# Performance work log

Measured on AMD Instinct MI355X. Metric: run time of the kernel, lower is better.

## Reference

```python
import jax, jax.numpy as jnp
import numpy as np

B, K, D = 16384, 512, 64

def _lin(k, fan_in, shape):
    return jax.random.normal(k, shape, jnp.float32) * (1.0 / np.sqrt(fan_in))

def setup_inputs() -> dict:
    key = jax.random.key(0)
    ks = jax.random.split(key, 12)
    return {
        'X':  jax.random.normal(ks[0], (B, 1, 28, 28), jnp.float32),
        'W1': _lin(ks[1], 784, (784, 1000)),  'b1': jnp.zeros((1000,), jnp.float32),
        'W2': _lin(ks[2], 1000, (1000, 500)), 'b2': jnp.zeros((500,), jnp.float32),
        'W3': _lin(ks[3], 500, (500, 300)),   'b3': jnp.zeros((300,), jnp.float32),
        'W4': _lin(ks[4], 300, (300, D)),     'b4': jnp.zeros((D,), jnp.float32),
        'E':  jax.random.normal(ks[5], (K, D), jnp.float32),
        'V1': _lin(ks[6], D, (D, 300)),       'c1': jnp.zeros((300,), jnp.float32),
        'V2': _lin(ks[7], 300, (300, 500)),   'c2': jnp.zeros((500,), jnp.float32),
        'V3': _lin(ks[8], 500, (500, 1000)),  'c3': jnp.zeros((1000,), jnp.float32),
        'V4': _lin(ks[9], 1000, (1000, 784)), 'c4': jnp.zeros((784,), jnp.float32),
    }

def find_nearest(query, target):
    # Euclidean nearest row of `target` for each row of `query`.
    # Expanded form ||q||^2 + ||t||^2 - 2 q.t ; argmin of d2 == argmin of sqrt(d2).
    d2 = (jnp.sum(query * query, axis=1, keepdims=True)
          + jnp.sum(target * target, axis=1)[None, :]
          - 2.0 * query @ target.T)                      # [Nq, Nt]
    idx = jnp.argmin(d2, axis=1)
    return target[idx]

def reference(X, W1, b1, W2, b2, W3, b3, W4, b4, E,
              V1, c1, V2, c2, V3, c3, V4, c4):
    x = X.reshape(-1, 784)
    h = jax.nn.relu(x @ W1 + b1)
    h = jax.nn.relu(h @ W2 + b2)
    h = jax.nn.relu(h @ W3 + b3)
    Z_enc = h @ W4 + b4                                   # [B, D]
    Z_dec = find_nearest(Z_enc, E)                        # [B, D] gathered codebook rows
    g = jax.nn.leaky_relu(Z_dec @ V1 + c1, 0.1)
    g = jax.nn.leaky_relu(g @ V2 + c2, 0.1)
    g = jax.nn.leaky_relu(g @ V3 + c3, 0.1)
    X_recon = jnp.tanh(g @ V4 + c4).reshape(-1, 1, 28, 28)
    Z_enc_for_embd = find_nearest(E, Z_enc)               # [K, D] gathered encoder rows
    return (X_recon, Z_enc, Z_dec, Z_enc_for_embd)
```

## Files before the change

kernel.cpp:

```cpp
#include <hip/hip_runtime.h>
#include <hip/hip_bf16.h>


typedef __attribute__((ext_vector_type(8))) short short8v;
typedef __attribute__((ext_vector_type(4))) float f32x4;

__device__ inline ushort f2bf(float v) {
    __hip_bfloat16 h = __float2bfloat16(v);
    return *reinterpret_cast<ushort*>(&h);
}
__device__ inline float bf2f(ushort s) {
    __hip_bfloat16 h;
    *reinterpret_cast<ushort*>(&h) = s;
    return __bfloat162float(h);
}

__device__ __forceinline__ void stage_tile(const ushort* __restrict__ src,
                                           ushort* dst, int wid, int lane)
{
#pragma unroll
    for (int j = 0; j < 2; ++j) {
        const int ci = (j << 2) + wid;
        __builtin_amdgcn_global_load_lds(
            (const __attribute__((address_space(1))) unsigned int*)(src + ci * 512 + lane * 8),
            (__attribute__((address_space(3))) unsigned int*)(dst + ci * 512),
            16, 0, 0);
    }
}

template<int ACT, bool SPLIT, int OMODE>
__global__ __launch_bounds__(256)
void gemm_mfma(const ushort* __restrict__ At, const ushort* __restrict__ Alt,
               const ushort* __restrict__ Bt, const ushort* __restrict__ Blt,
               const float* __restrict__ bias,
               float* __restrict__ Cf, ushort* __restrict__ Chi, ushort* __restrict__ Clo,
               int kbgA, int nsteps, int N)
{
    __shared__ short8v AhV[512];
    __shared__ short8v BhV[512];
    __shared__ short8v AlV[SPLIT ? 512 : 1];
    __shared__ short8v BlV[SPLIT ? 512 : 1];
    ushort* Ah = (ushort*)AhV;
    ushort* Bh = (ushort*)BhV;
    ushort* Al = (ushort*)AlV;
    ushort* Bl = (ushort*)BlV;

    const int tid  = threadIdx.x;
    const int lane = tid & 63;
    const int wid  = tid >> 6;
    const int wr   = (wid >> 1) * 64;
    const int wc   = (wid & 1) * 64;

    const int flat = blockIdx.y * gridDim.x + blockIdx.x;
    const int cpx  = (gridDim.x * gridDim.y) >> 3;
    const int swz  = (flat & 7) * cpx + (flat >> 3);
    const int cb   = swz % gridDim.x;
    const int rb   = swz / gridDim.x;
    const int row0 = rb * 128;
    const int col0 = cb * 128;

    f32x4 acc[4][4];
#pragma unroll
    for (int m = 0; m < 4; ++m)
#pragma unroll
        for (int n = 0; n < 4; ++n) acc[m][n] = (f32x4){0.f, 0.f, 0.f, 0.f};

    const int fr = lane & 15;
    const int kq = lane >> 4;

    const size_t abase = (size_t)rb * kbgA * 1024;
    const size_t bbase = (size_t)cb * kbgA * 1024;

    for (int s = 0; s < nsteps; ++s) {
        const size_t off = (size_t)s * 4096;
        stage_tile(At + abase + off, Ah, wid, lane);
        stage_tile(Bt + bbase + off, Bh, wid, lane);
        if (SPLIT) {
            stage_tile(Alt + abase + off, Al, wid, lane);
            stage_tile(Blt + bbase + off, Bl, wid, lane);
        }
        __syncthreads();

        short8v a_h[4], b_h[4], a_l[4], b_l[4];
#pragma unroll
        for (int m = 0; m < 4; ++m) {
            a_h[m] = *(const short8v*)&Ah[kq * 1024 + (wr + m * 16 + fr) * 8];
            if (SPLIT) a_l[m] = *(const short8v*)&Al[kq * 1024 + (wr + m * 16 + fr) * 8];
        }
#pragma unroll
        for (int n = 0; n < 4; ++n) {
            b_h[n] = *(const short8v*)&Bh[kq * 1024 + (wc + n * 16 + fr) * 8];
            if (SPLIT) b_l[n] = *(const short8v*)&Bl[kq * 1024 + (wc + n * 16 + fr) * 8];
        }
#pragma unroll
        for (int m = 0; m < 4; ++m)
#pragma unroll
            for (int n = 0; n < 4; ++n) {
                acc[m][n] = __builtin_amdgcn_mfma_f32_16x16x32_bf16(a_h[m], b_h[n], acc[m][n], 0, 0, 0);
                if (SPLIT) {
                    acc[m][n] = __builtin_amdgcn_mfma_f32_16x16x32_bf16(a_h[m], b_l[n], acc[m][n], 0, 0, 0);
                    acc[m][n] = __builtin_amdgcn_mfma_f32_16x16x32_bf16(a_l[m], b_h[n], acc[m][n], 0, 0, 0);
                }
            }
        __syncthreads();
    }

    const int kbgN = gridDim.x << 4;
#pragma unroll
    for (int n = 0; n < 4; ++n) {
        const int c = col0 + wc + n * 16 + fr;
        const float bv = (bias && c < N) ? bias[c] : 0.f;
#pragma unroll
        for (int m = 0; m < 4; ++m) {
#pragma unroll
            for (int i = 0; i < 4; ++i) {
                const int r = row0 + wr + m * 16 + kq * 4 + i;
                float v = acc[m][n][i] + bv;
                if (ACT == 1) v = fmaxf(v, 0.f);
                else if (ACT == 2) v = (v > 0.f) ? v : 0.1f * v;
                else if (ACT == 3) v = tanhf(v);
                if (OMODE == 0) {
                    if (c < N) Cf[(size_t)r * N + c] = v;
                } else {
                    if (c >= N) v = 0.f;
                    const size_t oi = (((size_t)(r >> 7) * kbgN + (c >> 3)) * 128 + (r & 127)) * 8 + (c & 7);
                    const ushort h = f2bf(v);
                    Chi[oi] = h;
                    if (OMODE == 2) Clo[oi] = f2bf(v - bf2f(h));
                }
            }
        }
    }
}

__global__ __launch_bounds__(256)
void gemm_f32_bt(const float* __restrict__ A, const float* __restrict__ W,
                 float* __restrict__ C, int M, int K, int N)
{
    __shared__ float As[16][68];
    __shared__ float Ws[16][68];

    const int tid = threadIdx.x;
    const int tx = tid & 15, ty = tid >> 4;
    const int row0 = blockIdx.y * 64, col0 = blockIdx.x * 64;

    float acc[4][4];
#pragma unroll
    for (int i = 0; i < 4; ++i)
#pragma unroll
        for (int j = 0; j < 4; ++j) acc[i][j] = 0.f;

    const int a_row = tid >> 2, a_k4 = (tid & 3) << 2;
    const int t_col = tid >> 2, t_k4 = (tid & 3) << 2;

    for (int k0 = 0; k0 < K; k0 += 16) {
        {
            const int gr = row0 + a_row, gk = k0 + a_k4;
            float4 av = *reinterpret_cast<const float4*>(A + (size_t)gr * K + gk);
            As[a_k4 + 0][a_row] = av.x; As[a_k4 + 1][a_row] = av.y;
            As[a_k4 + 2][a_row] = av.z; As[a_k4 + 3][a_row] = av.w;
        }
        {
            const int gc = col0 + t_col, gk = k0 + t_k4;
            float4 wv = *reinterpret_cast<const float4*>(W + (size_t)gc * K + gk);
            Ws[t_k4 + 0][t_col] = wv.x; Ws[t_k4 + 1][t_col] = wv.y;
            Ws[t_k4 + 2][t_col] = wv.z; Ws[t_k4 + 3][t_col] = wv.w;
        }
        __syncthreads();
#pragma unroll
        for (int kk = 0; kk < 16; ++kk) {
            float4 a = *reinterpret_cast<const float4*>(&As[kk][ty << 2]);
            float4 w = *reinterpret_cast<const float4*>(&Ws[kk][tx << 2]);
            acc[0][0] += a.x * w.x; acc[0][1] += a.x * w.y; acc[0][2] += a.x * w.z; acc[0][3] += a.x * w.w;
            acc[1][0] += a.y * w.x; acc[1][1] += a.y * w.y; acc[1][2] += a.y * w.z; acc[1][3] += a.y * w.w;
            acc[2][0] += a.z * w.x; acc[2][1] += a.z * w.y; acc[2][2] += a.z * w.z; acc[2][3] += a.z * w.w;
            acc[3][0] += a.w * w.x; acc[3][1] += a.w * w.y; acc[3][2] += a.w * w.z; acc[3][3] += a.w * w.w;
        }
        __syncthreads();
    }
#pragma unroll
    for (int i = 0; i < 4; ++i) {
        const int r = row0 + (ty << 2) + i;
#pragma unroll
        for (int j = 0; j < 4; ++j) {
            const int c = col0 + (tx << 2) + j;
            C[(size_t)r * N + c] = acc[i][j];
        }
    }
}

__global__ void row_norms64(const float* __restrict__ X, float* __restrict__ out, int rows)
{
    int r = blockIdx.x * blockDim.x + threadIdx.x;
    if (r >= rows) return;
    const float* p = X + (size_t)r * 64;
    float s = 0.f;
#pragma unroll
    for (int i = 0; i < 16; ++i) {
        float4 v = *reinterpret_cast<const float4*>(p + i * 4);
        s += v.x * v.x + v.y * v.y + v.z * v.z + v.w * v.w;
    }
    out[r] = s;
}

__global__ __launch_bounds__(256)
void argmin_rows(const float* __restrict__ S, const float* __restrict__ En2,
                 const float* __restrict__ E, float* __restrict__ Zdec,
                 ushort* __restrict__ Zdcb)
{
    const int wave = (blockIdx.x * blockDim.x + threadIdx.x) >> 6;
    const int lane = threadIdx.x & 63;
    if (wave >= 16384) return;
    const float* Srow = S + (size_t)wave * 512;
    float best = INFINITY;
    int bidx = 0x7fffffff;
    for (int k = lane; k < 512; k += 64) {
        float v = En2[k] - 2.0f * Srow[k];
        if (v < best) { best = v; bidx = k; }
    }
#pragma unroll
    for (int off = 32; off > 0; off >>= 1) {
        float ov = __shfl_down(best, off);
        int   oi = __shfl_down(bidx, off);
        if (ov < best || (ov == best && oi < bidx)) { best = ov; bidx = oi; }
    }
    bidx = __shfl(bidx, 0);
    const float val = E[(size_t)bidx * 64 + lane];
    Zdec[(size_t)wave * 64 + lane] = val;
    const size_t oi = (((size_t)(wave >> 7) * 8 + (lane >> 3)) * 128 + (wave & 127)) * 8 + (lane & 7);
    Zdcb[oi] = f2bf(val);
}

__global__ __launch_bounds__(256)
void argmin_cols_p1(const float* __restrict__ S, const float* __restrict__ Zn2,
                    float* __restrict__ pval, int* __restrict__ pidx)
{
    const int g   = blockIdx.x;
    const int tid = threadIdx.x;
    const int r0  = g << 6;
    float b0 = INFINITY, b1 = INFINITY;
    int   i0 = 0, i1 = 0;
    for (int r = 0; r < 64; ++r) {
        const float zn = Zn2[r0 + r];
        const float* row = S + (size_t)(r0 + r) * 512;
        const float v0 = zn - 2.0f * row[tid];
        const float v1 = zn - 2.0f * row[tid + 256];
        if (v0 < b0) { b0 = v0; i0 = r0 + r; }
        if (v1 < b1) { b1 = v1; i1 = r0 + r; }
    }
    pval[(size_t)tid * 256 + g]         = b0;
    pidx[(size_t)tid * 256 + g]         = i0;
    pval[(size_t)(tid + 256) * 256 + g] = b1;
    pidx[(size_t)(tid + 256) * 256 + g] = i1;
}

__global__ __launch_bounds__(256)
void argmin_cols_p2(const float* __restrict__ pval, const int* __restrict__ pidx,
                    const float* __restrict__ Zenc, float* __restrict__ Zemb)
{
    const int k   = blockIdx.x;
    const int tid = threadIdx.x;
    float v = pval[(size_t)k * 256 + tid];
    int   i = pidx[(size_t)k * 256 + tid];
    __shared__ float vs[256];
    __shared__ int   is_[256];
    vs[tid] = v; is_[tid] = i;
    __syncthreads();
    for (int s = 128; s > 0; s >>= 1) {
        if (tid < s) {
            if (vs[tid + s] < vs[tid] ||
                (vs[tid + s] == vs[tid] && is_[tid + s] < is_[tid])) {
                vs[tid] = vs[tid + s]; is_[tid] = is_[tid + s];
            }
        }
        __syncthreads();
    }
    const int idx = is_[0];
    if (tid < 64) Zemb[(size_t)k * 64 + tid] = Zenc[(size_t)idx * 64 + tid];
}

__global__ void conv_x(const float* __restrict__ X, ushort* __restrict__ hi,
                       ushort* __restrict__ lo)
{
    const long total = 128L * 100 * 1024;
    for (long idx = blockIdx.x * 256L + threadIdx.x; idx < total; idx += (long)gridDim.x * 256L) {
        const int j  = (int)(idx & 7);
        const long t = idx >> 3;
        const int rn = (int)(t & 127);
        const long u = t >> 7;
        const int kb = (int)(u % 100);
        const int rb = (int)(u / 100);
        const int r = rb * 128 + rn;
        const int k = kb * 8 + j;
        const float v = (k < 784) ? X[(size_t)r * 784 + k] : 0.f;
        const ushort h = f2bf(v);
        hi[idx] = h;
        lo[idx] = f2bf(v - bf2f(h));
    }
}

template<bool SPLIT>
__global__ void prep_w(const float* __restrict__ W, ushort* __restrict__ hi,
                       ushort* __restrict__ lo, int K, int N, int kbgTot, int npanels)
{
    const long total = (long)npanels * kbgTot * 1024;
    for (long idx = blockIdx.x * 256L + threadIdx.x; idx < total; idx += (long)gridDim.x * 256L) {
        const int j  = (int)(idx & 7);
        const long t = idx >> 3;
        const int cn = (int)(t & 127);
        const long u = t >> 7;
        const int kb = (int)(u % kbgTot);
        const int p  = (int)(u / kbgTot);
        const int k = kb * 8 + j;
        const int n = p * 128 + cn;
        const float v = (k < K && n < N) ? W[(size_t)k * N + n] : 0.f;
        const ushort h = f2bf(v);
        hi[idx] = h;
        if (SPLIT) lo[idx] = f2bf(v - bf2f(h));
    }
}

extern "C" void kernel_launch(void* const* d_in, const int* in_sizes, int n_in,
                              void* d_out, int out_size, void* d_ws, size_t ws_size,
                              hipStream_t stream)
{
    const float* X  = (const float*)d_in[0];
    const float* W1 = (const float*)d_in[1];
    const float* b1 = (const float*)d_in[2];
    const float* W2 = (const float*)d_in[3];
    const float* b2 = (const float*)d_in[4];
    const float* W3 = (const float*)d_in[5];
    const float* b3 = (const float*)d_in[6];
    const float* W4 = (const float*)d_in[7];
    const float* b4 = (const float*)d_in[8];
    const float* E  = (const float*)d_in[9];
    const float* V1 = (const float*)d_in[10];
    const float* c1 = (const float*)d_in[11];
    const float* V2 = (const float*)d_in[12];
    const float* c2 = (const float*)d_in[13];
    const float* V3 = (const float*)d_in[14];
    const float* c3 = (const float*)d_in[15];
    const float* V4 = (const float*)d_in[16];
    const float* c4 = (const float*)d_in[17];

    float* out  = (float*)d_out;
    float* Xrec = out;
    float* Zenc = out + 12845056;
    float* Zdec = out + 13893632;
    float* Zemb = out + 14942208;

    char* ws = (char*)d_ws;
    ushort* Xhi = (ushort*)(ws + 0);
    ushort* Xlo = (ushort*)(ws + 26214400);
    ushort* h2h = (ushort*)(ws + 0);
    ushort* h2l = (ushort*)(ws + 16777216);
    float*  S   = (float*)(ws + 0);
    ushort* g3  = (ushort*)(ws + 0);
    ushort* h1l = (ushort*)(ws + 52428800);
    ushort* h3h = (ushort*)(ws + 52428800);
    ushort* h3l = (ushort*)(ws + 65011712);
    ushort* g1  = (ushort*)(ws + 52428800);
    ushort* g2  = (ushort*)(ws + 65011712);
    ushort* h1h = (ushort*)d_out;
    float*  Zn2  = (float*)(ws + 85983232);
    float*  En2  = (float*)(ws + 86048768);
    ushort* Zdcb = (ushort*)(ws + 86050816);
    ushort* Wt1h = (ushort*)(ws + 88147968);
    ushort* Wt1l = (ushort*)(ws + 89786368);
    ushort* Wt2h = (ushort*)(ws + 91424768);
    ushort* Wt2l = (ushort*)(ws + 92473344);
    ushort* Wt3h = (ushort*)(ws + 93521920);
    ushort* Wt3l = (ushort*)(ws + 93915136);
    ushort* Wt4h = (ushort*)(ws + 94308352);
    ushort* Wt4l = (ushort*)(ws + 94406656);
    ushort* Vt1  = (ushort*)(ws + 94504960);
    ushort* Vt2  = (ushort*)(ws + 94554112);
    ushort* Vt3  = (ushort*)(ws + 94947328);
    ushort* Vt4  = (ushort*)(ws + 95995904);
    float*  Pv   = (float*)(ws + 97830912);
    int*    Pi   = (int*)  (ws + 98355200);

    const dim3 blk(256);

    conv_x<<<dim3(2048), blk, 0, stream>>>(X, Xhi, Xlo);
    prep_w<true ><<<dim3(256), blk, 0, stream>>>(W1, Wt1h, Wt1l, 784, 1000, 100, 8);
    prep_w<true ><<<dim3(256), blk, 0, stream>>>(W2, Wt2h, Wt2l, 1000, 500, 128, 4);
    prep_w<true ><<<dim3(128), blk, 0, stream>>>(W3, Wt3h, Wt3l, 500, 300, 64, 3);
    prep_w<true ><<<dim3(64),  blk, 0, stream>>>(W4, Wt4h, Wt4l, 300, 64, 48, 1);
    prep_w<false><<<dim3(64),  blk, 0, stream>>>(V1, Vt1, nullptr, 64, 300, 8, 3);
    prep_w<false><<<dim3(128), blk, 0, stream>>>(V2, Vt2, nullptr, 300, 500, 48, 4);
    prep_w<false><<<dim3(256), blk, 0, stream>>>(V3, Vt3, nullptr, 500, 1000, 64, 8);
    prep_w<false><<<dim3(256), blk, 0, stream>>>(V4, Vt4, nullptr, 1000, 784, 128, 7);

    gemm_mfma<1, true, 2><<<dim3(8, 128), blk, 0, stream>>>(Xhi, Xlo, Wt1h, Wt1l, b1, nullptr, h1h, h1l, 100, 25, 1000);
    gemm_mfma<1, true, 2><<<dim3(4, 128), blk, 0, stream>>>(h1h, h1l, Wt2h, Wt2l, b2, nullptr, h2h, h2l, 128, 32, 500);
    gemm_mfma<1, true, 2><<<dim3(3, 128), blk, 0, stream>>>(h2h, h2l, Wt3h, Wt3l, b3, nullptr, h3h, h3l, 64, 16, 300);
    gemm_mfma<0, true, 0><<<dim3(1, 128), blk, 0, stream>>>(h3h, h3l, Wt4h, Wt4l, b4, Zenc, nullptr, nullptr, 48, 12, 64);

    row_norms64<<<dim3(8),  dim3(64), 0, stream>>>(E,    En2, 512);
    row_norms64<<<dim3(64), blk,      0, stream>>>(Zenc, Zn2, 16384);
    gemm_f32_bt<<<dim3(8, 256), blk, 0, stream>>>(Zenc, E, S, 16384, 64, 512);
    argmin_rows<<<dim3(4096), blk, 0, stream>>>(S, En2, E, Zdec, Zdcb);
    argmin_cols_p1<<<dim3(256), blk, 0, stream>>>(S, Zn2, Pv, Pi);
    argmin_cols_p2<<<dim3(512), blk, 0, stream>>>(Pv, Pi, Zenc, Zemb);

    gemm_mfma<2, false, 1><<<dim3(3, 128), blk, 0, stream>>>(Zdcb, nullptr, Vt1, nullptr, c1, nullptr, g1, nullptr, 8, 2, 300);
    gemm_mfma<2, false, 1><<<dim3(4, 128), blk, 0, stream>>>(g1, nullptr, Vt2, nullptr, c2, nullptr, g2, nullptr, 48, 12, 500);
    gemm_mfma<2, false, 1><<<dim3(8, 128), blk, 0, stream>>>(g2, nullptr, Vt3, nullptr, c3, nullptr, g3, nullptr, 64, 16, 1000);
    gemm_mfma<3, false, 0><<<dim3(7, 128), blk, 0, stream>>>(g3, nullptr, Vt4, nullptr, c4, Xrec, nullptr, nullptr, 128, 32, 784);
}
```

Measured before the change: 569.1 us.

## Fuse distance GEMM and both argmin passes into one nearest-neighbor kernel

Replaces the separate fp32 distance GEMM, row argmin and column-argmin partial kernels with a single kernel that computes dot products per 64-row block and reduces both directions without materialising the 16384x512 score matrix. It also merges the eight weight-prep launches into one batched kernel with vectorised stores. This removes a large intermediate write/read and several launches, but the fused kernel runs only 256 blocks and does heavy per-codeword shuffle reductions, which may leave the GPU underoccupied.

```diff
diff --git a/kernel.cpp b/kernel.cpp
--- a/kernel.cpp
+++ b/kernel.cpp
@@ -133,62 +133,6 @@
     }
 }
 
-__global__ __launch_bounds__(256)
-void gemm_f32_bt(const float* __restrict__ A, const float* __restrict__ W,
-                 float* __restrict__ C, int M, int K, int N)
-{
-    __shared__ float As[16][68];
-    __shared__ float Ws[16][68];
-
-    const int tid = threadIdx.x;
-    const int tx = tid & 15, ty = tid >> 4;
-    const int row0 = blockIdx.y * 64, col0 = blockIdx.x * 64;
-
-    float acc[4][4];
-#pragma unroll
-    for (int i = 0; i < 4; ++i)
-#pragma unroll
-        for (int j = 0; j < 4; ++j) acc[i][j] = 0.f;
-
-    const int a_row = tid >> 2, a_k4 = (tid & 3) << 2;
-    const int t_col = tid >> 2, t_k4 = (tid & 3) << 2;
-
-    for (int k0 = 0; k0 < K; k0 += 16) {
-        {
-            const int gr = row0 + a_row, gk = k0 + a_k4;
-            float4 av = *reinterpret_cast<const float4*>(A + (size_t)gr * K + gk);
-            As[a_k4 + 0][a_row] = av.x; As[a_k4 + 1][a_row] = av.y;
-            As[a_k4 + 2][a_row] = av.z; As[a_k4 + 3][a_row] = av.w;
-        }
-        {
-            const int gc = col0 + t_col, gk = k0 + t_k4;
-            float4 wv = *reinterpret_cast<const float4*>(W + (size_t)gc * K + gk);
-            Ws[t_k4 + 0][t_col] = wv.x; Ws[t_k4 + 1][t_col] = wv.y;
-            Ws[t_k4 + 2][t_col] = wv.z; Ws[t_k4 + 3][t_col] = wv.w;
-        }
-        __syncthreads();
-#pragma unroll
-        for (int kk = 0; kk < 16; ++kk) {
-            float4 a = *reinterpret_cast<const float4*>(&As[kk][ty << 2]);
-            float4 w = *reinterpret_cast<const float4*>(&Ws[kk][tx << 2]);
-            acc[0][0] += a.x * w.x; acc[0][1] += a.x * w.y; acc[0][2] += a.x * w.z; acc[0][3] += a.x * w.w;
-            acc[1][0] += a.y * w.x; acc[1][1] += a.y * w.y; acc[1][2] += a.y * w.z; acc[1][3] += a.y * w.w;
-            acc[2][0] += a.z * w.x; acc[2][1] += a.z * w.y; acc[2][2] += a.z * w.z; acc[2][3] += a.z * w.w;
-            acc[3][0] += a.w * w.x; acc[3][1] += a.w * w.y; acc[3][2] += a.w * w.z; acc[3][3] += a.w * w.w;
-        }
-        __syncthreads();
-    }
-#pragma unroll
-    for (int i = 0; i < 4; ++i) {
-        const int r = row0 + (ty << 2) + i;
-#pragma unroll
-        for (int j = 0; j < 4; ++j) {
-            const int c = col0 + (tx << 2) + j;
-            C[(size_t)r * N + c] = acc[i][j];
-        }
-    }
-}
-
 __global__ void row_norms64(const float* __restrict__ X, float* __restrict__ out, int rows)
 {
     int r = blockIdx.x * blockDim.x + threadIdx.x;
@@ -204,54 +148,135 @@
 }
 
 __global__ __launch_bounds__(256)
-void argmin_rows(const float* __restrict__ S, const float* __restrict__ En2,
-                 const float* __restrict__ E, float* __restrict__ Zdec,
-                 ushort* __restrict__ Zdcb)
-{
-    const int wave = (blockIdx.x * blockDim.x + threadIdx.x) >> 6;
-    const int lane = threadIdx.x & 63;
-    if (wave >= 16384) return;
-    const float* Srow = S + (size_t)wave * 512;
-    float best = INFINITY;
-    int bidx = 0x7fffffff;
-    for (int k = lane; k < 512; k += 64) {
-        float v = En2[k] - 2.0f * Srow[k];
-        if (v < best) { best = v; bidx = k; }
-    }
-#pragma unroll
-    for (int off = 32; off > 0; off >>= 1) {
-        float ov = __shfl_down(best, off);
-        int   oi = __shfl_down(bidx, off);
-        if (ov < best || (ov == best && oi < bidx)) { best = ov; bidx = oi; }
-    }
-    bidx = __shfl(bidx, 0);
-    const float val = E[(size_t)bidx * 64 + lane];
-    Zdec[(size_t)wave * 64 + lane] = val;
-    const size_t oi = (((size_t)(wave >> 7) * 8 + (lane >> 3)) * 128 + (wave & 127)) * 8 + (lane & 7);
-    Zdcb[oi] = f2bf(val);
-}
-
-__global__ __launch_bounds__(256)
-void argmin_cols_p1(const float* __restrict__ S, const float* __restrict__ Zn2,
-                    float* __restrict__ pval, int* __restrict__ pidx)
-{
-    const int g   = blockIdx.x;
-    const int tid = threadIdx.x;
-    const int r0  = g << 6;
-    float b0 = INFINITY, b1 = INFINITY;
-    int   i0 = 0, i1 = 0;
-    for (int r = 0; r < 64; ++r) {
-        const float zn = Zn2[r0 + r];
-        const float* row = S + (size_t)(r0 + r) * 512;
-        const float v0 = zn - 2.0f * row[tid];
-        const float v1 = zn - 2.0f * row[tid + 256];
-        if (v0 < b0) { b0 = v0; i0 = r0 + r; }
-        if (v1 < b1) { b1 = v1; i1 = r0 + r; }
-    }
-    pval[(size_t)tid * 256 + g]         = b0;
-    pidx[(size_t)tid * 256 + g]         = i0;
-    pval[(size_t)(tid + 256) * 256 + g] = b1;
-    pidx[(size_t)(tid + 256) * 256 + g] = i1;
+void fused_nn(const float* __restrict__ Zenc, const float* __restrict__ E,
+              const float* __restrict__ En2,
+              float* __restrict__ Zdec, ushort* __restrict__ Zdcb,
+              float* __restrict__ Pv, int* __restrict__ Pi)
+{
+    const int b    = blockIdx.x;
+    const int r0   = b << 6;
+    const int tid  = threadIdx.x;
+    const int lane = tid & 63;
+    const int wu   = __builtin_amdgcn_readfirstlane(tid >> 6);
+
+    __shared__ float Zl[64][65];
+    __shared__ float rbv[4][64];
+    __shared__ int   rbi[4][64];
+    __shared__ int   widx[64];
+
+    {
+        const int r  = tid >> 2;
+        const int dq = (tid & 3) << 4;
+        const float* src = Zenc + (size_t)(r0 + r) * 64 + dq;
+#pragma unroll
+        for (int q = 0; q < 4; ++q) {
+            float4 v = *(const float4*)(src + q * 4);
+            Zl[r][dq + q * 4 + 0] = v.x;
+            Zl[r][dq + q * 4 + 1] = v.y;
+            Zl[r][dq + q * 4 + 2] = v.z;
+            Zl[r][dq + q * 4 + 3] = v.w;
+        }
+    }
+    __syncthreads();
+
+    float zn2 = 0.f;
+#pragma unroll
+    for (int d = 0; d < 64; ++d) zn2 += Zl[lane][d] * Zl[lane][d];
+
+    float rbest = INFINITY;
+    int   ridx  = 0x7fffffff;
+
+    for (int c0 = 0; c0 < 512; c0 += 128) {
+        const float* Ew = E + ((size_t)(c0 + (wu << 5)) << 6);
+
+        float dot[32];
+#pragma unroll
+        for (int ki = 0; ki < 32; ++ki) dot[ki] = 0.f;
+
+        for (int d0 = 0; d0 < 64; d0 += 16) {
+            float zc[16];
+#pragma unroll
+            for (int q = 0; q < 16; ++q) zc[q] = Zl[lane][d0 + q];
+#pragma unroll
+            for (int ki = 0; ki < 32; ++ki) {
+                const float4* er4 = (const float4*)(Ew + (ki << 6) + d0);
+                const float4 e0 = er4[0], e1 = er4[1], e2 = er4[2], e3 = er4[3];
+                dot[ki] = fmaf(zc[0],  e0.x, dot[ki]);
+                dot[ki] = fmaf(zc[1],  e0.y, dot[ki]);
+                dot[ki] = fmaf(zc[2],  e0.z, dot[ki]);
+                dot[ki] = fmaf(zc[3],  e0.w, dot[ki]);
+                dot[ki] = fmaf(zc[4],  e1.x, dot[ki]);
+                dot[ki] = fmaf(zc[5],  e1.y, dot[ki]);
+                dot[ki] = fmaf(zc[6],  e1.z, dot[ki]);
+                dot[ki] = fmaf(zc[7],  e1.w, dot[ki]);
+                dot[ki] = fmaf(zc[8],  e2.x, dot[ki]);
+                dot[ki] = fmaf(zc[9],  e2.y, dot[ki]);
+                dot[ki] = fmaf(zc[10], e2.z, dot[ki]);
+                dot[ki] = fmaf(zc[11], e2.w, dot[ki]);
+                dot[ki] = fmaf(zc[12], e3.x, dot[ki]);
+                dot[ki] = fmaf(zc[13], e3.y, dot[ki]);
+                dot[ki] = fmaf(zc[14], e3.z, dot[ki]);
+                dot[ki] = fmaf(zc[15], e3.w, dot[ki]);
+            }
+        }
+
+        float cbv = 0.f; int cbi = 0;
+#pragma unroll
+        for (int ki = 0; ki < 32; ++ki) {
+            const int k = c0 + (wu << 5) + ki;
+            const float vr = En2[k] - 2.0f * dot[ki];
+            if (vr < rbest) { rbest = vr; ridx = k; }
+            float vc = zn2 - 2.0f * dot[ki];
+            int   ic = r0 + lane;
+#pragma unroll
+            for (int off = 32; off > 0; off >>= 1) {
+                const float ov = __shfl_xor(vc, off);
+                const int   oi = __shfl_xor(ic, off);
+                if (ov < vc || (ov == vc && oi < ic)) { vc = ov; ic = oi; }
+            }
+            if (lane == ki) { cbv = vc; cbi = ic; }
+        }
+        if (lane < 32) {
+            const int k = c0 + (wu << 5) + lane;
+            Pv[(size_t)k * 256 + b] = cbv;
+            Pi[(size_t)k * 256 + b] = cbi;
+        }
+    }
+
+    rbv[tid >> 6][lane] = rbest;
+    rbi[tid >> 6][lane] = ridx;
+    __syncthreads();
+    if (tid < 64) {
+        float bv = rbv[0][tid]; int bi = rbi[0][tid];
+#pragma unroll
+        for (int w2 = 1; w2 < 4; ++w2) {
+            const float v = rbv[w2][tid];
+            const int   i = rbi[w2][tid];
+            if (v < bv || (v == bv && i < bi)) { bv = v; bi = i; }
+        }
+        widx[tid] = bi;
+    }
+    __syncthreads();
+
+    {
+        const int r  = tid >> 2;
+        const int dq = (tid & 3) << 4;
+        const int R  = r0 + r;
+        const float* src = E + (size_t)widx[r] * 64 + dq;
+#pragma unroll
+        for (int q = 0; q < 4; ++q) {
+            float4 v = *(const float4*)(src + q * 4);
+            float* dst = Zdec + (size_t)R * 64 + dq + q * 4;
+            *(float4*)dst = v;
+            const float vv[4] = {v.x, v.y, v.z, v.w};
+#pragma unroll
+            for (int e = 0; e < 4; ++e) {
+                const int d = dq + q * 4 + e;
+                const size_t oi = (((size_t)(R >> 7) * 8 + (d >> 3)) * 128 + (R & 127)) * 8 + (d & 7);
+                Zdcb[oi] = f2bf(vv[e]);
+            }
+        }
+    }
 }
 
 __global__ __launch_bounds__(256)
@@ -299,25 +324,47 @@
     }
 }
 
-template<bool SPLIT>
-__global__ void prep_w(const float* __restrict__ W, ushort* __restrict__ hi,
-                       ushort* __restrict__ lo, int K, int N, int kbgTot, int npanels)
-{
-    const long total = (long)npanels * kbgTot * 1024;
-    for (long idx = blockIdx.x * 256L + threadIdx.x; idx < total; idx += (long)gridDim.x * 256L) {
-        const int j  = (int)(idx & 7);
-        const long t = idx >> 3;
-        const int cn = (int)(t & 127);
-        const long u = t >> 7;
-        const int kb = (int)(u % kbgTot);
-        const int p  = (int)(u / kbgTot);
-        const int k = kb * 8 + j;
-        const int n = p * 128 + cn;
+struct PrepAll {
+    const float* W[8];
+    ushort* hi[8];
+    ushort* lo[8];
+    int K[8], N[8], kbg[8];
+    int blk0[9];
+};
+
+__global__ __launch_bounds__(256)
+void prep_all(PrepAll P)
+{
+    const int bid = blockIdx.x;
+    int s = 0;
+#pragma unroll
+    for (int i = 1; i < 8; ++i) if (bid >= P.blk0[i]) s = i;
+    const int  K = P.K[s], N = P.N[s], kbg = P.kbg[s];
+    const bool split = (s < 4);
+    const float* W = P.W[s];
+    ushort* hi = P.hi[s];
+    ushort* lo = P.lo[s];
+
+    const long idx = (long)(bid - P.blk0[s]) * 1024 + threadIdx.x * 4;
+    const int j0 = (int)(idx & 7);
+    const long t = idx >> 3;
+    const int cn = (int)(t & 127);
+    const long u = t >> 7;
+    const int kb = (int)(u % kbg);
+    const int p  = (int)(u / kbg);
+    const int n  = p * 128 + cn;
+
+    ushort hv[4], lv[4];
+#pragma unroll
+    for (int e = 0; e < 4; ++e) {
+        const int k = kb * 8 + j0 + e;
         const float v = (k < K && n < N) ? W[(size_t)k * N + n] : 0.f;
         const ushort h = f2bf(v);
-        hi[idx] = h;
-        if (SPLIT) lo[idx] = f2bf(v - bf2f(h));
-    }
+        hv[e] = h;
+        lv[e] = f2bf(v - bf2f(h));
+    }
+    *(ushort4*)&hi[idx] = *(ushort4*)hv;
+    if (split) *(ushort4*)&lo[idx] = *(ushort4*)lv;
 }
 
 extern "C" void kernel_launch(void* const* d_in, const int* in_sizes, int n_in,
@@ -354,7 +401,6 @@
     ushort* Xlo = (ushort*)(ws + 26214400);
     ushort* h2h = (ushort*)(ws + 0);
     ushort* h2l = (ushort*)(ws + 16777216);
-    float*  S   = (float*)(ws + 0);
     ushort* g3  = (ushort*)(ws + 0);
     ushort* h1l = (ushort*)(ws + 52428800);
     ushort* h3h = (ushort*)(ws + 52428800);
@@ -362,7 +408,6 @@
     ushort* g1  = (ushort*)(ws + 52428800);
     ushort* g2  = (ushort*)(ws + 65011712);
     ushort* h1h = (ushort*)d_out;
-    float*  Zn2  = (float*)(ws + 85983232);
     float*  En2  = (float*)(ws + 86048768);
     ushort* Zdcb = (ushort*)(ws + 86050816);
     ushort* Wt1h = (ushort*)(ws + 88147968);
@@ -383,25 +428,33 @@
     const dim3 blk(256);
 
     conv_x<<<dim3(2048), blk, 0, stream>>>(X, Xhi, Xlo);
-    prep_w<true ><<<dim3(256), blk, 0, stream>>>(W1, Wt1h, Wt1l, 784, 1000, 100, 8);
-    prep_w<true ><<<dim3(256), blk, 0, stream>>>(W2, Wt2h, Wt2l, 1000, 500, 128, 4);
-    prep_w<true ><<<dim3(128), blk, 0, stream>>>(W3, Wt3h, Wt3l, 500, 300, 64, 3);
-    prep_w<true ><<<dim3(64),  blk, 0, stream>>>(W4, Wt4h, Wt4l, 300, 64, 48, 1);
-    prep_w<false><<<dim3(64),  blk, 0, stream>>>(V1, Vt1, nullptr, 64, 300, 8, 3);
-    prep_w<false><<<dim3(128), blk, 0, stream>>>(V2, Vt2, nullptr, 300, 500, 48, 4);
-    prep_w<false><<<dim3(256), blk, 0, stream>>>(V3, Vt3, nullptr, 500, 1000, 64, 8);
-    prep_w<false><<<dim3(256), blk, 0, stream>>>(V4, Vt4, nullptr, 1000, 784, 128, 7);
+    {
+        PrepAll P;
+        const float* Wl[8] = {W1, W2, W3, W4, V1, V2, V3, V4};
+        ushort* Hl[8] = {Wt1h, Wt2h, Wt3h, Wt4h, Vt1, Vt2, Vt3, Vt4};
+        ushort* Ll[8] = {Wt1l, Wt2l, Wt3l, Wt4l, nullptr, nullptr, nullptr, nullptr};
+        const int Kl[8]   = {784, 1000, 500, 300, 64, 300, 500, 1000};
+        const int Nl[8]   = {1000, 500, 300, 64, 300, 500, 1000, 784};
+        const int KBl[8]  = {100, 128, 64, 48, 8, 48, 64, 128};
+        const int NPl[8]  = {8, 4, 3, 1, 3, 4, 8, 7};
+        int acc = 0;
+        for (int i = 0; i < 8; ++i) {
+            P.W[i] = Wl[i]; P.hi[i] = Hl[i]; P.lo[i] = Ll[i];
+            P.K[i] = Kl[i]; P.N[i] = Nl[i]; P.kbg[i] = KBl[i];
+            P.blk0[i] = acc;
+            acc += NPl[i] * KBl[i];
+        }
+        P.blk0[8] = acc;
+        prep_all<<<dim3(acc), blk, 0, stream>>>(P);
+    }
 
     gemm_mfma<1, true, 2><<<dim3(8, 128), blk, 0, stream>>>(Xhi, Xlo, Wt1h, Wt1l, b1, nullptr, h1h, h1l, 100, 25, 1000);
     gemm_mfma<1, true, 2><<<dim3(4, 128), blk, 0, stream>>>(h1h, h1l, Wt2h, Wt2l, b2, nullptr, h2h, h2l, 128, 32, 500);
     gemm_mfma<1, true, 2><<<dim3(3, 128), blk, 0, stream>>>(h2h, h2l, Wt3h, Wt3l, b3, nullptr, h3h, h3l, 64, 16, 300);
     gemm_mfma<0, true, 0><<<dim3(1, 128), blk, 0, stream>>>(h3h, h3l, Wt4h, Wt4l, b4, Zenc, nullptr, nullptr, 48, 12, 64);
 
-    row_norms64<<<dim3(8),  dim3(64), 0, stream>>>(E,    En2, 512);
-    row_norms64<<<dim3(64), blk,      0, stream>>>(Zenc, Zn2, 16384);
-    gemm_f32_bt<<<dim3(8, 256), blk, 0, stream>>>(Zenc, E, S, 16384, 64, 512);
-    argmin_rows<<<dim3(4096), blk, 0, stream>>>(S, En2, E, Zdec, Zdcb);
-    argmin_cols_p1<<<dim3(256), blk, 0, stream>>>(S, Zn2, Pv, Pi);
+    row_norms64<<<dim3(8), dim3(64), 0, stream>>>(E, En2, 512);
+    fused_nn<<<dim3(256), blk, 0, stream>>>(Zenc, E, En2, Zdec, Zdcb, Pv, Pi);
     argmin_cols_p2<<<dim3(512), blk, 0, stream>>>(Pv, Pi, Zenc, Zemb);
 
     gemm_mfma<2, false, 1><<<dim3(3, 128), blk, 0, stream>>>(Zdcb, nullptr, Vt1, nullptr, c1, nullptr, g1, nullptr, 8, 2, 300);
```

Result: slower. 693.6 us (+21.9%).
